# Optimization experiments

Measured on AMD Instinct MI355X. Metric: run time of the kernel, lower is better.

Reference implementation:

```python
import jax, jax.numpy as jnp
import numpy as np

INPUT_DIM, HIDDEN_DIM, OUTPUT_DIM = 64, 256, 64
# AutoNCP(256, 64): inter_and_command=192, command=int(0.4*192)=76, inter=116, motor=64
INTER, COMMAND, MOTOR = 116, 76, 64
SENSORY_FANOUT, INTER_FANOUT, MOTOR_FANIN = 58, 38, 38
B, T = 512, 256


def setup_inputs() -> dict:
    rng = np.random.default_rng(0)
    key = jax.random.key(0)
    d = {}
    # NCP wiring sparsity (binary masks; ncps takes abs() so polarity is irrelevant for the mask)
    m0 = np.zeros((INTER, INPUT_DIM), np.float32)
    for i in range(INPUT_DIM):
        m0[rng.choice(INTER, SENSORY_FANOUT, replace=False), i] = 1.0
    m1 = np.zeros((COMMAND, INTER), np.float32)
    for i in range(INTER):
        m1[rng.choice(COMMAND, INTER_FANOUT, replace=False), i] = 1.0
    m2 = np.zeros((MOTOR, COMMAND), np.float32)
    for o in range(MOTOR):
        m2[o, rng.choice(COMMAND, MOTOR_FANIN, replace=False)] = 1.0
    dims = [(INPUT_DIM, INTER, m0), (INTER, COMMAND, m1), (COMMAND, MOTOR, m2)]
    for l, (fi, h, m) in enumerate(dims):
        cat = fi + h
        # mask shape [h, fi+h]: sparse prev-layer block + all-ones recurrent block (as in WiredCfCCell)
        d[f"mask_{l}"] = jnp.asarray(np.concatenate([m, np.ones((h, h), np.float32)], axis=1))
        bound = float(1.0 / np.sqrt(cat))
        for nm in ("ff1", "ff2", "ta", "tb"):
            key, k1, k2 = jax.random.split(key, 3)
            d[f"w_{nm}_{l}"] = jax.random.uniform(k1, (h, cat), minval=-bound, maxval=bound, dtype=jnp.float32)
            d[f"b_{nm}_{l}"] = jax.random.uniform(k2, (h,), minval=-bound, maxval=bound, dtype=jnp.float32)
    key, k1, k2, kx = jax.random.split(key, 4)
    bound = float(1.0 / np.sqrt(OUTPUT_DIM))
    d["w_fc"] = jax.random.uniform(k1, (OUTPUT_DIM, OUTPUT_DIM), minval=-bound, maxval=bound, dtype=jnp.float32)
    d["b_fc"] = jax.random.uniform(k2, (OUTPUT_DIM,), minval=-bound, maxval=bound, dtype=jnp.float32)
    d["x"] = jax.random.normal(kx, (B, T, INPUT_DIM), dtype=jnp.float32)
    return d


def _cfc_cell(xin, h, w1, b1, w2, b2, wa, ba, wb, bb, mask):
    # CfCCell 'default' mode, no backbone, ts = 1.0
    cat = jnp.concatenate([xin, h], axis=-1)          # [B, fi+h]
    ff1 = jnp.tanh(cat @ (w1 * mask).T + b1)
    ff2 = jnp.tanh(cat @ (w2 * mask).T + b2)
    t_interp = jax.nn.sigmoid(cat @ wa.T + ba + cat @ wb.T + bb)  # sigmoid(t_a*1.0 + t_b)
    return ff1 * (1.0 - t_interp) + t_interp * ff2


def _forward(x, layer_params, masks, w_fc, b_fc):
    bsz = x.shape[0]
    h0 = tuple(jnp.zeros((bsz, h), x.dtype) for h in (INTER, COMMAND, MOTOR))

    def step(hs, xt):
        inp = xt
        new = []
        for l in range(3):  # inter -> command -> motor (structurally distinct layers)
            h = _cfc_cell(inp, hs[l], *layer_params[l], masks[l])
            inp = h
            new.append(h)
        return tuple(new), inp  # motor-layer output per step

    _, ys = jax.lax.scan(step, h0, jnp.swapaxes(x, 0, 1))
    y = jnp.swapaxes(ys, 0, 1)  # [B, T, MOTOR]
    return y @ w_fc.T + b_fc


def reference(x, w_ff1_0, b_ff1_0, w_ff2_0, b_ff2_0, w_ta_0, b_ta_0, w_tb_0, b_tb_0,
              w_ff1_1, b_ff1_1, w_ff2_1, b_ff2_1, w_ta_1, b_ta_1, w_tb_1, b_tb_1,
              w_ff1_2, b_ff1_2, w_ff2_2, b_ff2_2, w_ta_2, b_ta_2, w_tb_2, b_tb_2,
              w_fc, b_fc, mask_0, mask_1, mask_2):
    layer_params = [
        (w_ff1_0, b_ff1_0, w_ff2_0, b_ff2_0, w_ta_0, b_ta_0, w_tb_0, b_tb_0),
        (w_ff1_1, b_ff1_1, w_ff2_1, b_ff2_1, w_ta_1, b_ta_1, w_tb_1, b_tb_1),
        (w_ff1_2, b_ff1_2, w_ff2_2, b_ff2_2, w_ta_2, b_ta_2, w_tb_2, b_tb_2),
    ]
    return _forward(x, layer_params, (mask_0, mask_1, mask_2), w_fc, b_fc)
```

## Files before the change

### kernel.cpp

```cpp
#include <hip/hip_runtime.h>

typedef _Float16 f16x8 __attribute__((ext_vector_type(8)));
typedef _Float16 f16x4 __attribute__((ext_vector_type(4)));
typedef _Float16 f16x2 __attribute__((ext_vector_type(2)));
typedef float f32x4 __attribute__((ext_vector_type(4)));

#define NTH 1024
#define SEQT 256
#define LD0 200
#define LD1 200
#define LD2 168

struct KArgs { const float* in[30]; float* out; };

__device__ __forceinline__ float fast_tanh(float x) {
  return __fdividef(2.0f, 1.0f + __expf(-2.0f * x)) - 1.0f;
}
__device__ __forceinline__ float fast_sig(float x) {
  return __fdividef(1.0f, 1.0f + __expf(-x));
}

__device__ __forceinline__ f32x4 mfma16(f16x8 a, f16x8 b, f32x4 c) {
  return __builtin_amdgcn_mfma_f32_16x16x32_f16(a, b, c, 0, 0, 0);
}

__device__ __forceinline__ f16x4 combine3(const f32x4 acc[3]) {
  f16x4 v;
  #pragma unroll
  for (int q = 0; q < 4; ++q) {
    const float ff1 = fast_tanh(acc[0][q]);
    const float ff2 = fast_tanh(acc[1][q]);
    const float ti  = fast_sig(acc[2][q]);
    v[q] = (_Float16)(ff1 + ti * (ff2 - ff1));
  }
  return v;
}

template<int KT>
__device__ __forceinline__ void load_tile(f16x8* wW, const float* W1, const float* W2,
                                          const float* Wa, const float* Wb,
                                          const float* Mk, int n, int CAT, int H, int kb) {
  #pragma unroll
  for (int kt = 0; kt < KT; ++kt) {
    #pragma unroll
    for (int m = 0; m < 3; ++m) {
      f16x8 f;
      #pragma unroll
      for (int j = 0; j < 8; ++j) {
        const int k = kt * 32 + kb + j;
        float v = 0.f;
        if (n < H && k < CAT) {
          if (m == 0)      v = W1[n*CAT+k] * Mk[n*CAT+k];
          else if (m == 1) v = W2[n*CAT+k] * Mk[n*CAT+k];
          else             v = Wa[n*CAT+k] + Wb[n*CAT+k];
        }
        f[j] = (_Float16)v;
      }
      wW[m*KT + kt] = f;
    }
  }
}

template<int KT>
__device__ __forceinline__ void mma_tile_ld(f32x4 acc[3], const f16x8* wW,
                                            const _Float16* __restrict__ c,
                                            int LD, int r, int kb) {
  #pragma unroll
  for (int kt = 0; kt < KT; ++kt) {
    const f16x8 b = *reinterpret_cast<const f16x8*>(c + r*LD + kt*32 + kb);
    #pragma unroll
    for (int m = 0; m < 3; ++m)
      acc[m] = mfma16(wW[m*KT + kt], b, acc[m]);
  }
}

__device__ __forceinline__ void init3(f32x4 acc[3], const float* sb, int bs, int n0) {
  #pragma unroll
  for (int m = 0; m < 3; ++m)
    acc[m] = *reinterpret_cast<const f32x4*>(sb + m*bs + n0);
}

__device__ __forceinline__ f16x8 loadB8u(const _Float16* p) {
  const f16x4 a = *reinterpret_cast<const f16x4*>(p);
  const f16x4 b = *reinterpret_cast<const f16x4*>(p + 4);
  f16x8 v;
  v[0]=a[0]; v[1]=a[1]; v[2]=a[2]; v[3]=a[3];
  v[4]=b[0]; v[5]=b[1]; v[6]=b[2]; v[7]=b[3];
  return v;
}

__global__ __launch_bounds__(NTH, 4) void ncp_fused(KArgs args) {
  __shared__ __align__(16) _Float16 c0[2][16 * LD0];
  __shared__ __align__(16) _Float16 c1[2][16 * LD1];
  __shared__ __align__(16) _Float16 c2[2][16 * LD2];
  __shared__ __align__(16) _Float16 wt3[15 * 64 * 8];
  __shared__ __align__(16) _Float16 wfcs[8 * 64 * 8];
  __shared__ float b0s[3 * 128], b1s[3 * 80], b2s[3 * 64], bfcs[64];

  const int tid  = threadIdx.x;
  const int wv   = tid >> 6;
  const int lane = tid & 63;
  const int r    = lane & 15;
  const int g    = lane >> 4;
  const int kb   = g * 8;
  const int wgBase = blockIdx.x * 16;
  const float* __restrict__ xg = args.in[29];

  f16x8 wW[18];
  if (wv < 8) {
    load_tile<6>(wW, args.in[1], args.in[3], args.in[5], args.in[7], args.in[0],
                 wv*16 + r, 180, 116, kb);
  } else if (wv < 13) {
    load_tile<6>(wW, args.in[10], args.in[12], args.in[14], args.in[16], args.in[9],
                 (wv-8)*16 + r, 192, 76, kb);
  } else {
    load_tile<5>(wW, args.in[19], args.in[21], args.in[23], args.in[25], args.in[18],
                 (wv-13)*16 + r, 140, 64, kb);
  }

  for (int u = tid; u < 15 * 64; u += NTH) {
    const int ln = u & 63;
    const int ff = u >> 6;
    const int kt = ff % 5, m = ff / 5;
    const int n  = 48 + (ln & 15);
    const int kbb = (ln >> 4) * 8;
    f16x8 f;
    #pragma unroll
    for (int j = 0; j < 8; ++j) {
      const int k = kt*32 + kbb + j;
      float v = 0.f;
      if (k < 140) {
        if (m == 0)      v = args.in[19][n*140+k] * args.in[18][n*140+k];
        else if (m == 1) v = args.in[21][n*140+k] * args.in[18][n*140+k];
        else             v = args.in[23][n*140+k] + args.in[25][n*140+k];
      }
      f[j] = (_Float16)v;
    }
    *reinterpret_cast<f16x8*>(wt3 + (size_t)u * 8) = f;
  }
  for (int u = tid; u < 8 * 64; u += NTH) {
    const int ln = u & 63;
    const int ff = u >> 6;
    const int kt = ff & 1, ot = ff >> 1;
    f16x8 f;
    #pragma unroll
    for (int j = 0; j < 8; ++j)
      f[j] = (_Float16)args.in[27][(ot*16 + (ln & 15))*64 + kt*32 + (ln >> 4)*8 + j];
    *reinterpret_cast<f16x8*>(wfcs + (size_t)u * 8) = f;
  }
  if (tid < 128) {
    b0s[tid]       = (tid < 116) ? args.in[2][tid] : 0.f;
    b0s[128 + tid] = (tid < 116) ? args.in[4][tid] : 0.f;
    b0s[256 + tid] = (tid < 116) ? args.in[6][tid] + args.in[8][tid] : 0.f;
  }
  if (tid < 80) {
    b1s[tid]       = (tid < 76) ? args.in[11][tid] : 0.f;
    b1s[80 + tid]  = (tid < 76) ? args.in[13][tid] : 0.f;
    b1s[160 + tid] = (tid < 76) ? args.in[15][tid] + args.in[17][tid] : 0.f;
  }
  if (tid < 64) {
    b2s[tid]       = args.in[20][tid];
    b2s[64 + tid]  = args.in[22][tid];
    b2s[128 + tid] = args.in[24][tid] + args.in[26][tid];
    bfcs[tid]      = args.in[28][tid];
  }
  for (int i = tid; i < 2 * 16 * LD0; i += NTH) c0[0][i] = (_Float16)0.f;
  for (int i = tid; i < 2 * 16 * LD1; i += NTH) c1[0][i] = (_Float16)0.f;
  for (int i = tid; i < 2 * 16 * LD2; i += NTH) c2[0][i] = (_Float16)0.f;
  __syncthreads();
  const int rr = (tid & 511) >> 5, cc = (tid & 31) * 2;
  if (tid < 512) {
    const float2 v = *reinterpret_cast<const float2*>(
        xg + ((size_t)(wgBase + rr) * SEQT) * 64 + cc);
    f16x2 pk; pk[0] = (_Float16)v.x; pk[1] = (_Float16)v.y;
    *reinterpret_cast<f16x2*>(c0[0] + rr * LD0 + cc) = pk;
  }
  __syncthreads();

  const float* xp = xg + ((size_t)(wgBase + rr) * SEQT + 1) * 64 + cc;
  const int otb = (wv >= 13) ? (wv - 13) : 0;
  float* outp = args.out + ((size_t)(wgBase + r) * SEQT) * 64 + otb * 32 + 4 * g;

  #pragma unroll 1
  for (int p = 0; p < SEQT + 3; ++p) {
    const int cur = p & 1, nxt = cur ^ 1;

    float2 xv;
    const bool doX = (tid < 512) && (p < SEQT - 1);
    if (doX) xv = *reinterpret_cast<const float2*>(xp);

    if (wv < 8) {
      if (p < SEQT) {
        f32x4 a[3];
        const int nb = wv*16 + 4*g;
        init3(a, b0s, 128, nb);
        __builtin_amdgcn_s_setprio(1);
        mma_tile_ld<6>(a, wW, c0[cur], LD0, r, kb);
        __builtin_amdgcn_s_setprio(0);
        const f16x4 v = combine3(a);
        if (nb < 116) {
          *reinterpret_cast<f16x4*>(c1[nxt] + r*LD1 + nb)      = v;
          *reinterpret_cast<f16x4*>(c0[nxt] + r*LD0 + 64 + nb) = v;
        }
      }
    } else if (wv < 13) {
      if (p >= 1 && p <= SEQT) {
        f32x4 a[3];
        const int nb = (wv-8)*16 + 4*g;
        init3(a, b1s, 80, nb);
        __builtin_amdgcn_s_setprio(1);
        mma_tile_ld<6>(a, wW, c1[cur], LD1, r, kb);
        __builtin_amdgcn_s_setprio(0);
        const f16x4 v = combine3(a);
        if (nb < 76) {
          *reinterpret_cast<f16x4*>(c1[nxt] + r*LD1 + 116 + nb) = v;
          *reinterpret_cast<f16x4*>(c2[nxt] + r*LD2 + nb)       = v;
        }
      }
    } else if (wv < 15) {
      if (p >= 3) {
        const int ot0 = (wv - 13) * 2;
        f32x4 fa0 = *reinterpret_cast<const f32x4*>(bfcs + ot0*16 + 4*g);
        f32x4 fa1 = *reinterpret_cast<const f32x4*>(bfcs + ot0*16 + 16 + 4*g);
        const f16x8 hb0 = loadB8u(c2[cur] + r*LD2 + 76 + kb);
        const f16x8 hb1 = loadB8u(c2[cur] + r*LD2 + 76 + 32 + kb);
        const f16x8 wf00 = *reinterpret_cast<const f16x8*>(wfcs + (size_t)((ot0*2    )*64 + lane)*8);
        const f16x8 wf01 = *reinterpret_cast<const f16x8*>(wfcs + (size_t)((ot0*2 + 1)*64 + lane)*8);
        const f16x8 wf10 = *reinterpret_cast<const f16x8*>(wfcs + (size_t)((ot0*2 + 2)*64 + lane)*8);
        const f16x8 wf11 = *reinterpret_cast<const f16x8*>(wfcs + (size_t)((ot0*2 + 3)*64 + lane)*8);
        fa0 = mfma16(wf00, hb0, fa0); fa0 = mfma16(wf01, hb1, fa0);
        fa1 = mfma16(wf10, hb0, fa1); fa1 = mfma16(wf11, hb1, fa1);
        *reinterpret_cast<f32x4*>(outp)      = fa0;
        *reinterpret_cast<f32x4*>(outp + 16) = fa1;
        outp += 64;
      }
      if (p >= 2 && p <= SEQT + 1) {
        f32x4 a[3];
        const int nb = (wv-13)*16 + 4*g;
        init3(a, b2s, 64, nb);
        __builtin_amdgcn_s_setprio(1);
        mma_tile_ld<5>(a, wW, c2[cur], LD2, r, kb);
        __builtin_amdgcn_s_setprio(0);
        const f16x4 v = combine3(a);
        *reinterpret_cast<f16x4*>(c2[nxt] + r*LD2 + 76 + nb) = v;
      }
    } else {
      if (p >= 2 && p <= SEQT + 1) {
        f32x4 a2[3], a3[3];
        init3(a2, b2s, 64, 32 + 4*g);
        init3(a3, b2s, 64, 48 + 4*g);
        __builtin_amdgcn_s_setprio(1);
        #pragma unroll
        for (int kt = 0; kt < 5; ++kt) {
          const f16x8 b = *reinterpret_cast<const f16x8*>(c2[cur] + r*LD2 + kt*32 + kb);
          #pragma unroll
          for (int m = 0; m < 3; ++m) {
            a2[m] = mfma16(wW[m*5 + kt], b, a2[m]);
            const f16x8 af = *reinterpret_cast<const f16x8*>(
                wt3 + (size_t)((m*5 + kt)*64 + lane) * 8);
            a3[m] = mfma16(af, b, a3[m]);
          }
        }
        __builtin_amdgcn_s_setprio(0);
        const f16x4 v2 = combine3(a2);
        const f16x4 v3 = combine3(a3);
        *reinterpret_cast<f16x4*>(c2[nxt] + r*LD2 + 76 + 32 + 4*g) = v2;
        *reinterpret_cast<f16x4*>(c2[nxt] + r*LD2 + 76 + 48 + 4*g) = v3;
      }
    }

    if (doX) {
      f16x2 pk; pk[0] = (_Float16)xv.x; pk[1] = (_Float16)xv.y;
      *reinterpret_cast<f16x2*>(c0[nxt] + rr * LD0 + cc) = pk;
      xp += 64;
    }
    __syncthreads();
  }
}

extern "C" void kernel_launch(void* const* d_in, const int* in_sizes, int n_in,
                              void* d_out, int out_size, void* d_ws, size_t ws_size,
                              hipStream_t stream) {
  KArgs args;
  for (int i = 0; i < 30; ++i) args.in[i] = (const float*)d_in[i];
  args.out = (float*)d_out;
  ncp_fused<<<dim3(32), dim3(NTH), 0, stream>>>(args);
}
```

Before: 712.7 us.

## Keep biases in registers, unroll phases by two, use exp2 and packed fp16 conversion

The bias vectors move from shared-memory arrays into per-wave registers and are fed as the first MFMA accumulator input. The time loop is unrolled by two so the double-buffer indices become compile-time constants. Activations now use exp2 with pre-scaled constants and packed round-toward-zero fp16 conversion. The x staging moves to 128 threads loading float4 pairs instead of 512 threads loading float2. All of this trims per-step instruction count and LDS traffic on the serial recurrence, at the cost of more registers and a loop of 260 phases where 259 were needed (the extra phase is guarded off).

```diff
diff --git a/kernel.cpp b/kernel.cpp
--- a/kernel.cpp
+++ b/kernel.cpp
@@ -13,26 +13,37 @@
 
 struct KArgs { const float* in[30]; float* out; };
 
-__device__ __forceinline__ float fast_tanh(float x) {
-  return __fdividef(2.0f, 1.0f + __expf(-2.0f * x)) - 1.0f;
-}
-__device__ __forceinline__ float fast_sig(float x) {
-  return __fdividef(1.0f, 1.0f + __expf(-x));
-}
-
 __device__ __forceinline__ f32x4 mfma16(f16x8 a, f16x8 b, f32x4 c) {
   return __builtin_amdgcn_mfma_f32_16x16x32_f16(a, b, c, 0, 0, 0);
 }
 
-__device__ __forceinline__ f16x4 combine3(const f32x4 acc[3]) {
-  f16x4 v;
+__device__ __forceinline__ f16x2 cvt_pk(float x, float y) {
+  return __builtin_bit_cast(f16x2, __builtin_amdgcn_cvt_pkrtz(x, y));
+}
+
+__device__ __forceinline__ f16x4 combine_pack(const f32x4 a[3]) {
+  float h[4];
   #pragma unroll
   for (int q = 0; q < 4; ++q) {
-    const float ff1 = fast_tanh(acc[0][q]);
-    const float ff2 = fast_tanh(acc[1][q]);
-    const float ti  = fast_sig(acc[2][q]);
-    v[q] = (_Float16)(ff1 + ti * (ff2 - ff1));
-  }
+    const float ff1 = 1.0f - __fdividef(2.0f, 1.0f + __builtin_amdgcn_exp2f(2.885390082f * a[0][q]));
+    const float ff2 = 1.0f - __fdividef(2.0f, 1.0f + __builtin_amdgcn_exp2f(2.885390082f * a[1][q]));
+    const float ti  = __fdividef(1.0f, 1.0f + __builtin_amdgcn_exp2f(-1.442695041f * a[2][q]));
+    h[q] = ff1 + ti * (ff2 - ff1);
+  }
+  const f16x2 lo = cvt_pk(h[0], h[1]);
+  const f16x2 hi = cvt_pk(h[2], h[3]);
+  f16x4 v; v[0]=lo[0]; v[1]=lo[1]; v[2]=hi[0]; v[3]=hi[1];
+  return v;
+}
+
+__device__ __forceinline__ f16x8 pack8(const float4 v0, const float4 v1) {
+  const f16x2 a = cvt_pk(v0.x, v0.y);
+  const f16x2 b = cvt_pk(v0.z, v0.w);
+  const f16x2 c = cvt_pk(v1.x, v1.y);
+  const f16x2 d = cvt_pk(v1.z, v1.w);
+  f16x8 v;
+  v[0]=a[0]; v[1]=a[1]; v[2]=b[0]; v[3]=b[1];
+  v[4]=c[0]; v[5]=c[1]; v[6]=d[0]; v[7]=d[1];
   return v;
 }
 
@@ -62,22 +73,32 @@
 }
 
 template<int KT>
-__device__ __forceinline__ void mma_tile_ld(f32x4 acc[3], const f16x8* wW,
-                                            const _Float16* __restrict__ c,
-                                            int LD, int r, int kb) {
-  #pragma unroll
-  for (int kt = 0; kt < KT; ++kt) {
-    const f16x8 b = *reinterpret_cast<const f16x8*>(c + r*LD + kt*32 + kb);
-    #pragma unroll
-    for (int m = 0; m < 3; ++m)
-      acc[m] = mfma16(wW[m*KT + kt], b, acc[m]);
-  }
-}
-
-__device__ __forceinline__ void init3(f32x4 acc[3], const float* sb, int bs, int n0) {
-  #pragma unroll
-  for (int m = 0; m < 3; ++m)
-    acc[m] = *reinterpret_cast<const f32x4*>(sb + m*bs + n0);
+__device__ __forceinline__ void mma_b(f32x4 acc[3], const f16x8* wW, const f32x4 bias[3],
+                                      const _Float16* __restrict__ cbase) {
+  {
+    const f16x8 b = *reinterpret_cast<const f16x8*>(cbase);
+    #pragma unroll
+    for (int m = 0; m < 3; ++m) acc[m] = mfma16(wW[m*KT], b, bias[m]);
+  }
+  #pragma unroll
+  for (int kt = 1; kt < KT; ++kt) {
+    const f16x8 b = *reinterpret_cast<const f16x8*>(cbase + kt*32);
+    #pragma unroll
+    for (int m = 0; m < 3; ++m) acc[m] = mfma16(wW[m*KT + kt], b, acc[m]);
+  }
+}
+
+__device__ __forceinline__ f32x4 ldb4(const float* b, int n0, int H) {
+  f32x4 v;
+  #pragma unroll
+  for (int j = 0; j < 4; ++j) v[j] = (n0 + j < H) ? b[n0 + j] : 0.0f;
+  return v;
+}
+__device__ __forceinline__ f32x4 ldb4s(const float* ba, const float* bb, int n0, int H) {
+  f32x4 v;
+  #pragma unroll
+  for (int j = 0; j < 4; ++j) v[j] = (n0 + j < H) ? (ba[n0 + j] + bb[n0 + j]) : 0.0f;
+  return v;
 }
 
 __device__ __forceinline__ f16x8 loadB8u(const _Float16* p) {
@@ -95,7 +116,6 @@
   __shared__ __align__(16) _Float16 c2[2][16 * LD2];
   __shared__ __align__(16) _Float16 wt3[15 * 64 * 8];
   __shared__ __align__(16) _Float16 wfcs[8 * 64 * 8];
-  __shared__ float b0s[3 * 128], b1s[3 * 80], b2s[3 * 64], bfcs[64];
 
   const int tid  = threadIdx.x;
   const int wv   = tid >> 6;
@@ -103,6 +123,7 @@
   const int r    = lane & 15;
   const int g    = lane >> 4;
   const int kb   = g * 8;
+  const int n4g  = 4 * g;
   const int wgBase = blockIdx.x * 16;
   const float* __restrict__ xg = args.in[29];
 
@@ -116,6 +137,37 @@
   } else {
     load_tile<5>(wW, args.in[19], args.in[21], args.in[23], args.in[25], args.in[18],
                  (wv-13)*16 + r, 140, 64, kb);
+  }
+
+  f32x4 bias[3], bias2[3];
+  f32x4 fcb0 = {0.f,0.f,0.f,0.f}, fcb1 = {0.f,0.f,0.f,0.f};
+  #pragma unroll
+  for (int m = 0; m < 3; ++m) bias2[m] = f32x4{0.f,0.f,0.f,0.f};
+  if (wv < 8) {
+    const int n0 = wv*16 + n4g;
+    bias[0] = ldb4(args.in[2], n0, 116);
+    bias[1] = ldb4(args.in[4], n0, 116);
+    bias[2] = ldb4s(args.in[6], args.in[8], n0, 116);
+  } else if (wv < 13) {
+    const int n0 = (wv-8)*16 + n4g;
+    bias[0] = ldb4(args.in[11], n0, 76);
+    bias[1] = ldb4(args.in[13], n0, 76);
+    bias[2] = ldb4s(args.in[15], args.in[17], n0, 76);
+  } else {
+    const int n0 = (wv-13)*16 + n4g;
+    bias[0] = ldb4(args.in[20], n0, 64);
+    bias[1] = ldb4(args.in[22], n0, 64);
+    bias[2] = ldb4s(args.in[24], args.in[26], n0, 64);
+    if (wv == 15) {
+      const int n3 = 48 + n4g;
+      bias2[0] = ldb4(args.in[20], n3, 64);
+      bias2[1] = ldb4(args.in[22], n3, 64);
+      bias2[2] = ldb4s(args.in[24], args.in[26], n3, 64);
+    } else {
+      const int ot0 = (wv-13)*2;
+      fcb0 = *reinterpret_cast<const f32x4*>(&args.in[28][ot0*16 + n4g]);
+      fcb1 = *reinterpret_cast<const f32x4*>(&args.in[28][ot0*16 + 16 + n4g]);
+    }
   }
 
   for (int u = tid; u < 15 * 64; u += NTH) {
@@ -148,134 +200,117 @@
       f[j] = (_Float16)args.in[27][(ot*16 + (ln & 15))*64 + kt*32 + (ln >> 4)*8 + j];
     *reinterpret_cast<f16x8*>(wfcs + (size_t)u * 8) = f;
   }
-  if (tid < 128) {
-    b0s[tid]       = (tid < 116) ? args.in[2][tid] : 0.f;
-    b0s[128 + tid] = (tid < 116) ? args.in[4][tid] : 0.f;
-    b0s[256 + tid] = (tid < 116) ? args.in[6][tid] + args.in[8][tid] : 0.f;
-  }
-  if (tid < 80) {
-    b1s[tid]       = (tid < 76) ? args.in[11][tid] : 0.f;
-    b1s[80 + tid]  = (tid < 76) ? args.in[13][tid] : 0.f;
-    b1s[160 + tid] = (tid < 76) ? args.in[15][tid] + args.in[17][tid] : 0.f;
-  }
-  if (tid < 64) {
-    b2s[tid]       = args.in[20][tid];
-    b2s[64 + tid]  = args.in[22][tid];
-    b2s[128 + tid] = args.in[24][tid] + args.in[26][tid];
-    bfcs[tid]      = args.in[28][tid];
-  }
   for (int i = tid; i < 2 * 16 * LD0; i += NTH) c0[0][i] = (_Float16)0.f;
   for (int i = tid; i < 2 * 16 * LD1; i += NTH) c1[0][i] = (_Float16)0.f;
   for (int i = tid; i < 2 * 16 * LD2; i += NTH) c2[0][i] = (_Float16)0.f;
   __syncthreads();
-  const int rr = (tid & 511) >> 5, cc = (tid & 31) * 2;
-  if (tid < 512) {
-    const float2 v = *reinterpret_cast<const float2*>(
-        xg + ((size_t)(wgBase + rr) * SEQT) * 64 + cc);
-    f16x2 pk; pk[0] = (_Float16)v.x; pk[1] = (_Float16)v.y;
-    *reinterpret_cast<f16x2*>(c0[0] + rr * LD0 + cc) = pk;
-  }
+
+  const int xi   = (tid >= 896) ? (tid - 896) : 0;
+  const int xrow = xi >> 3;
+  const int xcol = (xi & 7) * 8;
+  const float* xp = xg + ((size_t)(wgBase + xrow) * SEQT) * 64 + xcol;
+  if (tid >= 896) {
+    const float4 v0 = *reinterpret_cast<const float4*>(xp);
+    const float4 v1 = *reinterpret_cast<const float4*>(xp + 4);
+    *reinterpret_cast<f16x8*>(&c0[0][xrow * LD0 + xcol]) = pack8(v0, v1);
+  }
+  xp += 64;
   __syncthreads();
 
-  const float* xp = xg + ((size_t)(wgBase + rr) * SEQT + 1) * 64 + cc;
+  const int nb0 = wv*16 + n4g;
+  const int nb1 = (wv-8)*16 + n4g;
+  const int nb2 = (wv-13)*16 + n4g;
   const int otb = (wv >= 13) ? (wv - 13) : 0;
-  float* outp = args.out + ((size_t)(wgBase + r) * SEQT) * 64 + otb * 32 + 4 * g;
+  float* outp = args.out + ((size_t)(wgBase + r) * SEQT) * 64 + otb * 32 + n4g;
+
+#define PHASE(P, CUR, NXT) do {                                                 \
+    const int p_ = (P);                                                         \
+    float4 xv0, xv1;                                                            \
+    const bool doX = (tid >= 896) && (p_ < SEQT - 1);                           \
+    if (doX) { xv0 = *reinterpret_cast<const float4*>(xp);                      \
+               xv1 = *reinterpret_cast<const float4*>(xp + 4); }                \
+    if (wv < 8) {                                                               \
+      if (p_ < SEQT) {                                                          \
+        f32x4 a[3];                                                             \
+        __builtin_amdgcn_s_setprio(1);                                          \
+        mma_b<6>(a, wW, bias, &c0[CUR][r*LD0 + kb]);                            \
+        __builtin_amdgcn_s_setprio(0);                                          \
+        const f16x4 v = combine_pack(a);                                        \
+        if (nb0 < 116) {                                                        \
+          *reinterpret_cast<f16x4*>(&c1[NXT][r*LD1 + nb0])      = v;            \
+          *reinterpret_cast<f16x4*>(&c0[NXT][r*LD0 + 64 + nb0]) = v;            \
+        }                                                                       \
+      }                                                                         \
+    } else if (wv < 13) {                                                       \
+      if (p_ >= 1 && p_ <= SEQT) {                                              \
+        f32x4 a[3];                                                             \
+        __builtin_amdgcn_s_setprio(1);                                          \
+        mma_b<6>(a, wW, bias, &c1[CUR][r*LD1 + kb]);                            \
+        __builtin_amdgcn_s_setprio(0);                                          \
+        const f16x4 v = combine_pack(a);                                        \
+        if (nb1 < 76) {                                                         \
+          *reinterpret_cast<f16x4*>(&c1[NXT][r*LD1 + 116 + nb1]) = v;           \
+          *reinterpret_cast<f16x4*>(&c2[NXT][r*LD2 + nb1])       = v;           \
+        }                                                                       \
+      }                                                                         \
+    } else if (wv < 15) {                                                       \
+      if (p_ >= 3 && p_ <= SEQT + 2) {                                          \
+        f32x4 fa0 = fcb0, fa1 = fcb1;                                           \
+        const f16x8 hb0 = loadB8u(&c2[CUR][r*LD2 + 76 + kb]);                   \
+        const f16x8 hb1 = loadB8u(&c2[CUR][r*LD2 + 76 + 32 + kb]);              \
+        const f16x8 wf00 = *reinterpret_cast<const f16x8*>(&wfcs[((size_t)((otb*4    )*64 + lane))*8]); \
+        const f16x8 wf01 = *reinterpret_cast<const f16x8*>(&wfcs[((size_t)((otb*4 + 1)*64 + lane))*8]); \
+        const f16x8 wf10 = *reinterpret_cast<const f16x8*>(&wfcs[((size_t)((otb*4 + 2)*64 + lane))*8]); \
+        const f16x8 wf11 = *reinterpret_cast<const f16x8*>(&wfcs[((size_t)((otb*4 + 3)*64 + lane))*8]); \
+        fa0 = mfma16(wf00, hb0, fa0); fa0 = mfma16(wf01, hb1, fa0);             \
+        fa1 = mfma16(wf10, hb0, fa1); fa1 = mfma16(wf11, hb1, fa1);             \
+        *reinterpret_cast<f32x4*>(outp)      = fa0;                             \
+        *reinterpret_cast<f32x4*>(outp + 16) = fa1;                             \
+        outp += 64;                                                             \
+      }                                                                         \
+      if (p_ >= 2 && p_ <= SEQT + 1) {                                          \
+        f32x4 a[3];                                                             \
+        __builtin_amdgcn_s_setprio(1);                                          \
+        mma_b<5>(a, wW, bias, &c2[CUR][r*LD2 + kb]);                            \
+        __builtin_amdgcn_s_setprio(0);                                          \
+        const f16x4 v = combine_pack(a);                                        \
+        *reinterpret_cast<f16x4*>(&c2[NXT][r*LD2 + 76 + nb2]) = v;              \
+      }                                                                         \
+    } else {                                                                    \
+      if (p_ >= 2 && p_ <= SEQT + 1) {                                          \
+        f32x4 a2[3], a3[3];                                                     \
+        __builtin_amdgcn_s_setprio(1);                                          \
+        _Pragma("unroll")                                                       \
+        for (int kt = 0; kt < 5; ++kt) {                                        \
+          const f16x8 b = *reinterpret_cast<const f16x8*>(&c2[CUR][r*LD2 + kt*32 + kb]); \
+          _Pragma("unroll")                                                     \
+          for (int m = 0; m < 3; ++m) {                                         \
+            a2[m] = mfma16(wW[m*5 + kt], b, (kt == 0) ? bias[m] : a2[m]);       \
+            const f16x8 af = *reinterpret_cast<const f16x8*>(&wt3[((size_t)((m*5 + kt)*64 + lane))*8]); \
+            a3[m] = mfma16(af, b, (kt == 0) ? bias2[m] : a3[m]);                \
+          }                                                                     \
+        }                                                                       \
+        __builtin_amdgcn_s_setprio(0);                                          \
+        const f16x4 v2 = combine_pack(a2);                                      \
+        const f16x4 v3 = combine_pack(a3);                                      \
+        *reinterpret_cast<f16x4*>(&c2[NXT][r*LD2 + 76 + 32 + n4g]) = v2;        \
+        *reinterpret_cast<f16x4*>(&c2[NXT][r*LD2 + 76 + 48 + n4g]) = v3;        \
+      }                                                                         \
+    }                                                                           \
+    if (doX) {                                                                  \
+      *reinterpret_cast<f16x8*>(&c0[NXT][xrow * LD0 + xcol]) = pack8(xv0, xv1); \
+      xp += 64;                                                                 \
+    }                                                                           \
+    __syncthreads();                                                            \
+  } while (0)
 
   #pragma unroll 1
-  for (int p = 0; p < SEQT + 3; ++p) {
-    const int cur = p & 1, nxt = cur ^ 1;
-
-    float2 xv;
-    const bool doX = (tid < 512) && (p < SEQT - 1);
-    if (doX) xv = *reinterpret_cast<const float2*>(xp);
-
-    if (wv < 8) {
-      if (p < SEQT) {
-        f32x4 a[3];
-        const int nb = wv*16 + 4*g;
-        init3(a, b0s, 128, nb);
-        __builtin_amdgcn_s_setprio(1);
-        mma_tile_ld<6>(a, wW, c0[cur], LD0, r, kb);
-        __builtin_amdgcn_s_setprio(0);
-        const f16x4 v = combine3(a);
-        if (nb < 116) {
-          *reinterpret_cast<f16x4*>(c1[nxt] + r*LD1 + nb)      = v;
-          *reinterpret_cast<f16x4*>(c0[nxt] + r*LD0 + 64 + nb) = v;
-        }
-      }
-    } else if (wv < 13) {
-      if (p >= 1 && p <= SEQT) {
-        f32x4 a[3];
-        const int nb = (wv-8)*16 + 4*g;
-        init3(a, b1s, 80, nb);
-        __builtin_amdgcn_s_setprio(1);
-        mma_tile_ld<6>(a, wW, c1[cur], LD1, r, kb);
-        __builtin_amdgcn_s_setprio(0);
-        const f16x4 v = combine3(a);
-        if (nb < 76) {
-          *reinterpret_cast<f16x4*>(c1[nxt] + r*LD1 + 116 + nb) = v;
-          *reinterpret_cast<f16x4*>(c2[nxt] + r*LD2 + nb)       = v;
-        }
-      }
-    } else if (wv < 15) {
-      if (p >= 3) {
-        const int ot0 = (wv - 13) * 2;
-        f32x4 fa0 = *reinterpret_cast<const f32x4*>(bfcs + ot0*16 + 4*g);
-        f32x4 fa1 = *reinterpret_cast<const f32x4*>(bfcs + ot0*16 + 16 + 4*g);
-        const f16x8 hb0 = loadB8u(c2[cur] + r*LD2 + 76 + kb);
-        const f16x8 hb1 = loadB8u(c2[cur] + r*LD2 + 76 + 32 + kb);
-        const f16x8 wf00 = *reinterpret_cast<const f16x8*>(wfcs + (size_t)((ot0*2    )*64 + lane)*8);
-        const f16x8 wf01 = *reinterpret_cast<const f16x8*>(wfcs + (size_t)((ot0*2 + 1)*64 + lane)*8);
-        const f16x8 wf10 = *reinterpret_cast<const f16x8*>(wfcs + (size_t)((ot0*2 + 2)*64 + lane)*8);
-        const f16x8 wf11 = *reinterpret_cast<const f16x8*>(wfcs + (size_t)((ot0*2 + 3)*64 + lane)*8);
-        fa0 = mfma16(wf00, hb0, fa0); fa0 = mfma16(wf01, hb1, fa0);
-        fa1 = mfma16(wf10, hb0, fa1); fa1 = mfma16(wf11, hb1, fa1);
-        *reinterpret_cast<f32x4*>(outp)      = fa0;
-        *reinterpret_cast<f32x4*>(outp + 16) = fa1;
-        outp += 64;
-      }
-      if (p >= 2 && p <= SEQT + 1) {
-        f32x4 a[3];
-        const int nb = (wv-13)*16 + 4*g;
-        init3(a, b2s, 64, nb);
-        __builtin_amdgcn_s_setprio(1);
-        mma_tile_ld<5>(a, wW, c2[cur], LD2, r, kb);
-        __builtin_amdgcn_s_setprio(0);
-        const f16x4 v = combine3(a);
-        *reinterpret_cast<f16x4*>(c2[nxt] + r*LD2 + 76 + nb) = v;
-      }
-    } else {
-      if (p >= 2 && p <= SEQT + 1) {
-        f32x4 a2[3], a3[3];
-        init3(a2, b2s, 64, 32 + 4*g);
-        init3(a3, b2s, 64, 48 + 4*g);
-        __builtin_amdgcn_s_setprio(1);
-        #pragma unroll
-        for (int kt = 0; kt < 5; ++kt) {
-          const f16x8 b = *reinterpret_cast<const f16x8*>(c2[cur] + r*LD2 + kt*32 + kb);
-          #pragma unroll
-          for (int m = 0; m < 3; ++m) {
-            a2[m] = mfma16(wW[m*5 + kt], b, a2[m]);
-            const f16x8 af = *reinterpret_cast<const f16x8*>(
-                wt3 + (size_t)((m*5 + kt)*64 + lane) * 8);
-            a3[m] = mfma16(af, b, a3[m]);
-          }
-        }
-        __builtin_amdgcn_s_setprio(0);
-        const f16x4 v2 = combine3(a2);
-        const f16x4 v3 = combine3(a3);
-        *reinterpret_cast<f16x4*>(c2[nxt] + r*LD2 + 76 + 32 + 4*g) = v2;
-        *reinterpret_cast<f16x4*>(c2[nxt] + r*LD2 + 76 + 48 + 4*g) = v3;
-      }
-    }
-
-    if (doX) {
-      f16x2 pk; pk[0] = (_Float16)xv.x; pk[1] = (_Float16)xv.y;
-      *reinterpret_cast<f16x2*>(c0[nxt] + rr * LD0 + cc) = pk;
-      xp += 64;
-    }
-    __syncthreads();
-  }
+  for (int pp = 0; pp < (SEQT + 4) / 2; ++pp) {
+    const int p0 = pp * 2;
+    PHASE(p0,     0, 1);
+    PHASE(p0 + 1, 1, 0);
+  }
+#undef PHASE
 }
 
 extern "C" void kernel_launch(void* const* d_in, const int* in_sizes, int n_in,
```

New measurement: 980.4 us. 37.6% more time.
